# Optimization experiments

Hardware: AMD Instinct MI355X
Metric: run time of the kernel (lower is better)

## Reference

```python
import jax, jax.numpy as jnp
import numpy as np

# ---- JPEG constants ----
_Y_TABLE = np.array([
    [16, 11, 10, 16, 24, 40, 51, 61],
    [12, 12, 14, 19, 26, 58, 60, 55],
    [14, 13, 16, 24, 40, 57, 69, 56],
    [14, 17, 22, 29, 51, 87, 80, 62],
    [18, 22, 37, 56, 68, 109, 103, 77],
    [24, 35, 55, 64, 81, 104, 113, 92],
    [49, 64, 78, 87, 103, 121, 120, 101],
    [72, 92, 95, 98, 112, 100, 103, 99]], dtype=np.float32)
_C_TABLE = np.full((8, 8), 99.0, dtype=np.float32)
_C_TABLE[:4, :4] = np.array([
    [17, 18, 24, 47],
    [18, 21, 26, 66],
    [24, 26, 56, 99],
    [47, 66, 99, 99]], dtype=np.float32)

_i = np.arange(8, dtype=np.float64)
_T = (np.cos((2 * _i[:, None, None, None] + 1) * _i[None, None, :, None] * np.pi / 16)
      * np.cos((2 * _i[None, :, None, None] + 1) * _i[None, None, None, :] * np.pi / 16))
_alpha = np.ones(8); _alpha[0] = 1.0 / np.sqrt(2.0)
DCT_T = jnp.asarray(_T, jnp.float32)
DCT_SCALE = jnp.asarray(np.outer(_alpha, _alpha) * 0.25, jnp.float32)
IDCT_ALPHA = jnp.asarray(np.outer(_alpha, _alpha), jnp.float32)
Y_T = jnp.asarray(_Y_TABLE)
C_T = jnp.asarray(_C_TABLE)


def _split_blocks(c):
    # [N,H,W] -> [N, (H//8)*(W//8), 8, 8]
    N, H, W = c.shape
    return c.reshape(N, H // 8, 8, W // 8, 8).transpose(0, 1, 3, 2, 4).reshape(N, -1, 8, 8)


def _merge_blocks(b, H, W):
    N = b.shape[0]
    return b.reshape(N, H // 8, W // 8, 8, 8).transpose(0, 1, 3, 2, 4).reshape(N, H, W)


def _dct8x8(b):
    return DCT_SCALE * jnp.einsum('nbxy,xyuv->nbuv', b - 128.0, DCT_T)


def _idct8x8(b):
    return 0.25 * jnp.einsum('nbuv,xyuv->nbxy', b * IDCT_ALPHA, DCT_T) + 128.0


def _diff_round(x):
    r = jnp.round(x)
    return r + (x - r) ** 3


def _quality_to_factor(q):
    return (5000.0 / q if q < 50 else 200.0 - 2.0 * q) / 100.0


def _diff_jpeg(x, quality=99.0):
    # x: [N,3,16,16] roughly in [0,1]
    factor = _quality_to_factor(quality)
    img = x * 255.0
    M = jnp.array([[0.299, 0.587, 0.114],
                   [-0.168736, -0.331264, 0.5],
                   [0.5, -0.418688, -0.081312]], jnp.float32)
    shift = jnp.array([0.0, 128.0, 128.0], jnp.float32)
    ycc = jnp.einsum('nchw,kc->nkhw', img, M) + shift[None, :, None, None]
    y, cb, cr = ycc[:, 0], ycc[:, 1], ycc[:, 2]
    N, H, W = y.shape
    sub = lambda c: c.reshape(N, H // 2, 2, W // 2, 2).mean(axis=(2, 4))  # 2x2 chroma subsample

    def codec(c, tab):
        q = _diff_round(_dct8x8(_split_blocks(c)) / (tab * factor))
        return _idct8x8(q * (tab * factor))

    y2 = _merge_blocks(codec(y, Y_T), H, W)
    up = lambda c: jnp.repeat(jnp.repeat(c, 2, axis=1), 2, axis=2)
    cb2 = up(_merge_blocks(codec(sub(cb), C_T), H // 2, W // 2))
    cr2 = up(_merge_blocks(codec(sub(cr), C_T), H // 2, W // 2))
    ycc2 = jnp.stack([y2, cb2, cr2], axis=1)
    Mi = jnp.array([[1.0, 0.0, 1.402],
                    [1.0, -0.344136, -0.714136],
                    [1.0, 1.772, 0.0]], jnp.float32)
    shift2 = jnp.array([0.0, -128.0, -128.0], jnp.float32)
    rgb = jnp.einsum('nkhw,ck->nchw', ycc2 + shift2[None, :, None, None], Mi)
    return jnp.clip(rgb, 0.0, 255.0) / 255.0


def setup_inputs() -> dict:
    key = jax.random.key(0)
    x = jax.random.normal(key, (32, 1024, 14, 14), dtype=jnp.float32)
    return {"x": x}


def reference(x):
    orig_min = jnp.min(x, axis=(-2, -1), keepdims=True)
    orig_max = jnp.max(x, axis=(-2, -1), keepdims=True)
    rng = orig_max - orig_min + 1e-5
    xn = (x - orig_min) / rng
    B, C, H, W = x.shape
    # replicate each channel into a 3-channel image
    xr = jnp.broadcast_to(xn[:, :, None], (B, C, 3, H, W)).reshape(B * C, 3, H, W)
    xp = jnp.pad(xr, ((0, 0), (0, 0), (1, 1), (1, 1)), mode='edge')  # 14x14 -> 16x16
    comp = _diff_jpeg(xp, 99.0)
    comp = comp[:, :, 1:-1, 1:-1].reshape(B, C, 3, H, W).mean(axis=2)
    return comp * rng + orig_min
```

## Files before the change

kernel.cpp:

```cpp
#include <hip/hip_runtime.h>


namespace {

constexpr int CH_PER_WG = 8;
constexpr int HW        = 196;
constexpr int CH_STRIDE = 264;

constexpr float CM[8][8] = {
  { 0.35355339059327376f,  0.35355339059327376f,  0.35355339059327376f,  0.35355339059327376f,
    0.35355339059327376f,  0.35355339059327376f,  0.35355339059327376f,  0.35355339059327376f},
  { 0.49039264020161522f,  0.41573480615127262f,  0.27778511650980114f,  0.09754516100806417f,
   -0.09754516100806417f, -0.27778511650980114f, -0.41573480615127262f, -0.49039264020161522f},
  { 0.46193976625564337f,  0.19134171618254492f, -0.19134171618254492f, -0.46193976625564337f,
   -0.46193976625564337f, -0.19134171618254492f,  0.19134171618254492f,  0.46193976625564337f},
  { 0.41573480615127262f, -0.09754516100806417f, -0.49039264020161522f, -0.27778511650980114f,
    0.27778511650980114f,  0.49039264020161522f,  0.09754516100806417f, -0.41573480615127262f},
  { 0.35355339059327376f, -0.35355339059327376f, -0.35355339059327376f,  0.35355339059327376f,
    0.35355339059327376f, -0.35355339059327376f, -0.35355339059327376f,  0.35355339059327376f},
  { 0.27778511650980114f, -0.49039264020161522f,  0.09754516100806417f,  0.41573480615127262f,
   -0.41573480615127262f, -0.09754516100806417f,  0.49039264020161522f, -0.27778511650980114f},
  { 0.19134171618254492f, -0.46193976625564337f,  0.46193976625564337f, -0.19134171618254492f,
   -0.19134171618254492f,  0.46193976625564337f, -0.46193976625564337f,  0.19134171618254492f},
  { 0.09754516100806417f, -0.27778511650980114f,  0.41573480615127262f, -0.49039264020161522f,
    0.49039264020161522f, -0.41573480615127262f,  0.27778511650980114f, -0.09754516100806417f},
};

}

__device__ const float YQTAB[8][8] = {
  {16,11,10,16,24,40,51,61},
  {12,12,14,19,26,58,60,55},
  {14,13,16,24,40,57,69,56},
  {14,17,22,29,51,87,80,62},
  {18,22,37,56,68,109,103,77},
  {24,35,55,64,81,104,113,92},
  {49,64,78,87,103,121,120,101},
  {72,92,95,98,112,100,103,99},
};

__global__ __launch_bounds__(256)
void jpeg_codec_kernel(const float* __restrict__ x, float* __restrict__ out, int ntot) {
  __shared__ float s_raw[CH_PER_WG * HW];
  __shared__ float s_bufA[CH_PER_WG * CH_STRIDE];
  __shared__ float s_bufB[CH_PER_WG * CH_STRIDE];
  __shared__ float s_min[CH_PER_WG];
  __shared__ float s_rng[CH_PER_WG];

  const int tid = threadIdx.x;
  const long long base = (long long)blockIdx.x * (CH_PER_WG * HW);
  const int lim = (int)min((long long)(CH_PER_WG * HW), (long long)ntot - base);

  #pragma unroll
  for (int k = 0; k < 7; ++k) {
    int idx = tid + k * 256;
    if (idx < lim) s_raw[idx] = x[base + idx];
  }
  __syncthreads();

  const int ch = tid >> 5;
  const int l  = tid & 31;

  {
    float vmin = 1e30f, vmax = -1e30f;
    for (int idx = l; idx < HW; idx += 32) {
      float v = s_raw[ch * HW + idx];
      vmin = fminf(vmin, v);
      vmax = fmaxf(vmax, v);
    }
    #pragma unroll
    for (int off = 16; off; off >>= 1) {
      vmin = fminf(vmin, __shfl_xor(vmin, off, 64));
      vmax = fmaxf(vmax, __shfl_xor(vmax, off, 64));
    }
    if (l == 0) { s_min[ch] = vmin; s_rng[ch] = vmax - vmin + 1e-5f; }
  }
  __syncthreads();

  {
    const float mn  = s_min[ch];
    const float rng = s_rng[ch];
    #pragma unroll
    for (int k = 0; k < 8; ++k) {
      int p  = l + 32 * k;
      int pr = p >> 4, pc = p & 15;
      int sr = pr - 1; sr = sr < 0 ? 0 : (sr > 13 ? 13 : sr);
      int sc = pc - 1; sc = sc < 0 ? 0 : (sc > 13 ? 13 : sc);
      float v = (s_raw[ch * HW + sr * 14 + sc] - mn) / rng * 255.0f - 128.0f;
      int b = ((pr >> 3) << 1) | (pc >> 3);
      s_bufA[ch * CH_STRIDE + b * 64 + (pr & 7) * 8 + (pc & 7)] = v;
    }
  }
  __syncthreads();

  const int b    = l >> 3;
  const int i    = l & 7;
  const int src0 = ch * CH_STRIDE + b * 64 + i * 8;
  const int dst0 = ch * CH_STRIDE + b * 64 + i;

  float m[8];

  #pragma unroll
  for (int j = 0; j < 8; ++j) m[j] = s_bufA[src0 + j];
  #pragma unroll
  for (int k = 0; k < 8; ++k) {
    float s = 0.0f;
    #pragma unroll
    for (int j = 0; j < 8; ++j) s = fmaf(m[j], CM[k][j], s);
    s_bufB[dst0 + 8 * k] = s;
  }
  __syncthreads();

  #pragma unroll
  for (int j = 0; j < 8; ++j) m[j] = s_bufB[src0 + j];
  #pragma unroll
  for (int k = 0; k < 8; ++k) {
    float s = 0.0f;
    #pragma unroll
    for (int j = 0; j < 8; ++j) s = fmaf(m[j], CM[k][j], s);
    float qv = YQTAB[k][i] * 0.02f;
    float xq = s / qv;
    float r  = rintf(xq);
    float e  = xq - r;
    s_bufA[dst0 + 8 * k] = (r + e * e * e) * qv;
  }
  __syncthreads();

  #pragma unroll
  for (int j = 0; j < 8; ++j) m[j] = s_bufA[src0 + j];
  #pragma unroll
  for (int k = 0; k < 8; ++k) {
    float s = 0.0f;
    #pragma unroll
    for (int j = 0; j < 8; ++j) s = fmaf(m[j], CM[j][k], s);
    s_bufB[dst0 + 8 * k] = s;
  }
  __syncthreads();

  #pragma unroll
  for (int j = 0; j < 8; ++j) m[j] = s_bufB[src0 + j];
  #pragma unroll
  for (int k = 0; k < 8; ++k) {
    float s = 0.0f;
    #pragma unroll
    for (int j = 0; j < 8; ++j) s = fmaf(m[j], CM[j][k], s);
    s_bufA[dst0 + 8 * k] = s;
  }
  __syncthreads();

  #pragma unroll
  for (int k = 0; k < 7; ++k) {
    int idx = tid + k * 256;
    if (idx < lim) {
      int c2  = idx / HW;
      int rem = idx - c2 * HW;
      int r   = rem / 14;
      int c   = rem - r * 14;
      int pr  = r + 1, pc = c + 1;
      int bb  = ((pr >> 3) << 1) | (pc >> 3);
      float v = s_bufA[c2 * CH_STRIDE + bb * 64 + (pr & 7) * 8 + (pc & 7)] + 128.0f;
      v = v < 0.0f ? 0.0f : (v > 255.0f ? 255.0f : v);
      out[base + idx] = (v / 255.0f) * s_rng[c2] + s_min[c2];
    }
  }
}

extern "C" void kernel_launch(void* const* d_in, const int* in_sizes, int n_in,
                              void* d_out, int out_size, void* d_ws, size_t ws_size,
                              hipStream_t stream) {
  const float* x = (const float*)d_in[0];
  float* out     = (float*)d_out;
  const int ntot = in_sizes[0];
  const int nch  = ntot / HW;
  const int grid = (nch + CH_PER_WG - 1) / CH_PER_WG;
  hipLaunchKernelGGL(jpeg_codec_kernel, dim3(grid), dim3(256), 0, stream,
                     x, out, ntot);
}
```

Baseline: 92.81 us.

## Vectorize global IO, fuse padding into first DCT pass, use wave-local LDS sync

Loads and stores use float4, and edge padding plus normalization are fused into the first row-DCT pass, removing a staging pass and two barriers. Block-wide barriers between DCT passes become s_waitcnt lgkmcnt(0), which relies on each channel being handled inside a single wavefront. The LDS block stride is padded to 9 to reduce bank conflicts in the transposed accesses. The float4 path assumes aligned bases and drops partial tail vectors when the total size is not a multiple of four.

Result: faster. 88.76 us (-4.4%).

```diff
diff --git a/kernel.cpp b/kernel.cpp
--- a/kernel.cpp
+++ b/kernel.cpp
@@ -5,7 +5,7 @@
 
 constexpr int CH_PER_WG = 8;
 constexpr int HW        = 196;
-constexpr int CH_STRIDE = 264;
+constexpr int CS        = 288;
 
 constexpr float CM[8][8] = {
   { 0.35355339059327376f,  0.35355339059327376f,  0.35355339059327376f,  0.35355339059327376f,
@@ -39,11 +39,13 @@
   {72,92,95,98,112,100,103,99},
 };
 
+#define WAVE_LDS_SYNC() asm volatile("s_waitcnt lgkmcnt(0)" ::: "memory")
+
 __global__ __launch_bounds__(256)
 void jpeg_codec_kernel(const float* __restrict__ x, float* __restrict__ out, int ntot) {
-  __shared__ float s_raw[CH_PER_WG * HW];
-  __shared__ float s_bufA[CH_PER_WG * CH_STRIDE];
-  __shared__ float s_bufB[CH_PER_WG * CH_STRIDE];
+  __shared__ __align__(16) float s_raw[CH_PER_WG * HW];
+  __shared__ float s_bufA[CH_PER_WG * CS];
+  __shared__ float s_bufB[CH_PER_WG * CS];
   __shared__ float s_min[CH_PER_WG];
   __shared__ float s_rng[CH_PER_WG];
 
@@ -51,68 +53,71 @@
   const long long base = (long long)blockIdx.x * (CH_PER_WG * HW);
   const int lim = (int)min((long long)(CH_PER_WG * HW), (long long)ntot - base);
 
-  #pragma unroll
-  for (int k = 0; k < 7; ++k) {
-    int idx = tid + k * 256;
-    if (idx < lim) s_raw[idx] = x[base + idx];
+  {
+    const float4* x4 = (const float4*)(x + base);
+    float4* r4 = (float4*)s_raw;
+    #pragma unroll
+    for (int k = 0; k < 2; ++k) {
+      int t = tid + k * 256;
+      if (t * 4 + 3 < lim + 1 && t < (CH_PER_WG * HW) / 4) r4[t] = x4[t];
+    }
   }
   __syncthreads();
 
   const int ch = tid >> 5;
   const int l  = tid & 31;
 
+  float mn, rng;
   {
     float vmin = 1e30f, vmax = -1e30f;
-    for (int idx = l; idx < HW; idx += 32) {
-      float v = s_raw[ch * HW + idx];
-      vmin = fminf(vmin, v);
-      vmax = fmaxf(vmax, v);
+    const float4* c4 = (const float4*)(s_raw + ch * HW);
+    #pragma unroll
+    for (int k = 0; k < 2; ++k) {
+      int t = l + k * 32;
+      if (t < HW / 4) {
+        float4 v = c4[t];
+        vmin = fminf(fminf(vmin, v.x), fminf(v.y, fminf(v.z, v.w)));
+        vmax = fmaxf(fmaxf(vmax, v.x), fmaxf(v.y, fmaxf(v.z, v.w)));
+      }
     }
     #pragma unroll
     for (int off = 16; off; off >>= 1) {
       vmin = fminf(vmin, __shfl_xor(vmin, off, 64));
       vmax = fmaxf(vmax, __shfl_xor(vmax, off, 64));
     }
-    if (l == 0) { s_min[ch] = vmin; s_rng[ch] = vmax - vmin + 1e-5f; }
+    mn  = vmin;
+    rng = vmax - vmin + 1e-5f;
+    if (l == 0) { s_min[ch] = mn; s_rng[ch] = rng; }
   }
-  __syncthreads();
 
-  {
-    const float mn  = s_min[ch];
-    const float rng = s_rng[ch];
-    #pragma unroll
-    for (int k = 0; k < 8; ++k) {
-      int p  = l + 32 * k;
-      int pr = p >> 4, pc = p & 15;
-      int sr = pr - 1; sr = sr < 0 ? 0 : (sr > 13 ? 13 : sr);
-      int sc = pc - 1; sc = sc < 0 ? 0 : (sc > 13 ? 13 : sc);
-      float v = (s_raw[ch * HW + sr * 14 + sc] - mn) / rng * 255.0f - 128.0f;
-      int b = ((pr >> 3) << 1) | (pc >> 3);
-      s_bufA[ch * CH_STRIDE + b * 64 + (pr & 7) * 8 + (pc & 7)] = v;
-    }
-  }
-  __syncthreads();
-
-  const int b    = l >> 3;
-  const int i    = l & 7;
-  const int src0 = ch * CH_STRIDE + b * 64 + i * 8;
-  const int dst0 = ch * CH_STRIDE + b * 64 + i;
+  const int b = l >> 3;
+  const int i = l & 7;
+  const int rbase = ch * CS + b * 72 + i * 9;
+  const int wbase = ch * CS + b * 72 + i;
 
   float m[8];
 
-  #pragma unroll
-  for (int j = 0; j < 8; ++j) m[j] = s_bufA[src0 + j];
-  #pragma unroll
-  for (int k = 0; k < 8; ++k) {
-    float s = 0.0f;
+  {
+    const int pr = ((b >> 1) << 3) + i;
+    int sr = pr - 1; sr = sr < 0 ? 0 : (sr > 13 ? 13 : sr);
+    const float* rp = s_raw + ch * HW + sr * 14;
     #pragma unroll
-    for (int j = 0; j < 8; ++j) s = fmaf(m[j], CM[k][j], s);
-    s_bufB[dst0 + 8 * k] = s;
+    for (int j = 0; j < 8; ++j) {
+      int pc = ((b & 1) << 3) + j - 1; pc = pc < 0 ? 0 : (pc > 13 ? 13 : pc);
+      m[j] = (rp[pc] - mn) / rng * 255.0f - 128.0f;
+    }
+    #pragma unroll
+    for (int k = 0; k < 8; ++k) {
+      float s = 0.0f;
+      #pragma unroll
+      for (int j = 0; j < 8; ++j) s = fmaf(m[j], CM[k][j], s);
+      s_bufB[wbase + 9 * k] = s;
+    }
   }
-  __syncthreads();
+  WAVE_LDS_SYNC();
 
   #pragma unroll
-  for (int j = 0; j < 8; ++j) m[j] = s_bufB[src0 + j];
+  for (int j = 0; j < 8; ++j) m[j] = s_bufB[rbase + j];
   #pragma unroll
   for (int k = 0; k < 8; ++k) {
     float s = 0.0f;
@@ -122,45 +127,56 @@
     float xq = s / qv;
     float r  = rintf(xq);
     float e  = xq - r;
-    s_bufA[dst0 + 8 * k] = (r + e * e * e) * qv;
+    s_bufA[wbase + 9 * k] = (r + e * e * e) * qv;
   }
-  __syncthreads();
+  WAVE_LDS_SYNC();
 
   #pragma unroll
-  for (int j = 0; j < 8; ++j) m[j] = s_bufA[src0 + j];
+  for (int j = 0; j < 8; ++j) m[j] = s_bufA[rbase + j];
   #pragma unroll
   for (int k = 0; k < 8; ++k) {
     float s = 0.0f;
     #pragma unroll
     for (int j = 0; j < 8; ++j) s = fmaf(m[j], CM[j][k], s);
-    s_bufB[dst0 + 8 * k] = s;
+    s_bufB[wbase + 9 * k] = s;
   }
-  __syncthreads();
+  WAVE_LDS_SYNC();
 
   #pragma unroll
-  for (int j = 0; j < 8; ++j) m[j] = s_bufB[src0 + j];
+  for (int j = 0; j < 8; ++j) m[j] = s_bufB[rbase + j];
   #pragma unroll
   for (int k = 0; k < 8; ++k) {
     float s = 0.0f;
     #pragma unroll
     for (int j = 0; j < 8; ++j) s = fmaf(m[j], CM[j][k], s);
-    s_bufA[dst0 + 8 * k] = s;
+    s_bufA[wbase + 9 * k] = s;
   }
   __syncthreads();
 
-  #pragma unroll
-  for (int k = 0; k < 7; ++k) {
-    int idx = tid + k * 256;
-    if (idx < lim) {
-      int c2  = idx / HW;
-      int rem = idx - c2 * HW;
-      int r   = rem / 14;
-      int c   = rem - r * 14;
-      int pr  = r + 1, pc = c + 1;
-      int bb  = ((pr >> 3) << 1) | (pc >> 3);
-      float v = s_bufA[c2 * CH_STRIDE + bb * 64 + (pr & 7) * 8 + (pc & 7)] + 128.0f;
-      v = v < 0.0f ? 0.0f : (v > 255.0f ? 255.0f : v);
-      out[base + idx] = (v / 255.0f) * s_rng[c2] + s_min[c2];
+  {
+    float4* o4 = (float4*)(out + base);
+    #pragma unroll
+    for (int k = 0; k < 2; ++k) {
+      int t = tid + k * 256;
+      if (t < (CH_PER_WG * HW) / 4 && t * 4 + 3 < lim + 1) {
+        int idx = 4 * t;
+        int c2  = idx / HW;
+        int rem = idx - c2 * HW;
+        int r0  = rem / 14, c0 = rem - 14 * r0;
+        float cmn = s_min[c2], crng = s_rng[c2];
+        float vals[4];
+        #pragma unroll
+        for (int q = 0; q < 4; ++q) {
+          int rr = r0, cc = c0 + q;
+          if (cc >= 14) { cc -= 14; ++rr; }
+          int pr = rr + 1, pc = cc + 1;
+          int bb = ((pr >> 3) << 1) | (pc >> 3);
+          float v = s_bufA[c2 * CS + bb * 72 + (pr & 7) * 9 + (pc & 7)] + 128.0f;
+          v = v < 0.0f ? 0.0f : (v > 255.0f ? 255.0f : v);
+          vals[q] = v / 255.0f * crng + cmn;
+        }
+        o4[t] = make_float4(vals[0], vals[1], vals[2], vals[3]);
+      }
     }
   }
 }
```
